# Performance work log

Measured on AMD Instinct MI355X. Metric: run time of the kernel, lower is better.

Reference implementation:

```python
import jax, jax.numpy as jnp
import numpy as np

B = 16384
ED = 32          # embed_dim
NF = 16          # num_filters
KS = [1, 3, 5, 7, 9]
LENS = {"pep": 12, "a1": 7, "a2": 8, "a3": 22, "b1": 6, "b2": 7, "b3": 23}


def setup_inputs() -> dict:
    key = jax.random.key(0)
    keys = jax.random.split(key, 32)
    ki = iter(keys)
    inp = {}
    for name, L in LENS.items():
        inp[name] = jax.random.normal(next(ki), (B, ED, L), dtype=jnp.float32)
    # conv weights: one stack of 7 convs per kernel size; w{k}: [7, NF, ED, k], bias c{k}: [7, NF]
    for k in KS:
        fan_in = ED * k
        bound = 1.0 / np.sqrt(fan_in)
        inp[f"w{k}"] = jax.random.uniform(next(ki), (7, NF, ED, k), jnp.float32, -bound, bound)
        inp[f"c{k}"] = jax.random.uniform(next(ki), (7, NF), jnp.float32, -bound, bound)
    dbound = 1.0 / np.sqrt(NF * 35)
    inp["dw"] = jax.random.uniform(next(ki), (NF * 35, 1), jnp.float32, -dbound, dbound)
    inp["db"] = jax.random.uniform(next(ki), (1,), jnp.float32, -dbound, dbound)
    return inp


def _branch(x, w, b):
    # x: [B, ED, L], w: [NF, ED, k], b: [NF] -> [B, NF] (conv 'same' + relu + global max)
    y = jax.lax.conv_general_dilated(x, w, window_strides=(1,), padding="SAME",
                                     dimension_numbers=("NCH", "OIH", "NCH"))
    y = jax.nn.relu(y + b[None, :, None])
    return jnp.max(y, axis=2)


def reference(pep, a1, a2, a3, b1, b2, b3, w1, w3, w5, w7, w9, c1, c3, c5, c7, c9, dw, db):
    xs = [pep, a1, a2, a3, b1, b2, b3]
    ws = {1: w1, 3: w3, 5: w5, 7: w7, 9: w9}
    cs = {1: c1, 3: c3, 5: c5, 7: c7, 9: c9}
    feats = []
    for i, x in enumerate(xs):  # fixed 7 inputs
        for k in KS:            # fixed 5 kernel sizes
            feats.append(_branch(x, ws[k][i], cs[k][i]))
    feat = jnp.concatenate(feats, axis=1)        # [B, 35*NF]
    out = jax.nn.sigmoid(feat @ dw + db)         # [B, 1]
    return jnp.squeeze(out, axis=-1)             # [B]
```

## Files before the change

### kernel.cpp

```cpp
#include <hip/hip_runtime.h>
#include <cmath>

namespace {

using bf16x8 = __attribute__((ext_vector_type(8))) short;
using f32x4  = __attribute__((ext_vector_type(4))) float;

constexpr int NT = 192;
constexpr int NS = 16;
constexpr int LPAD = 31;
constexpr int TILE_BYTES = NS * LPAD * 32 * 2;

__device__ __forceinline__ short f2bf(float f) {
  unsigned u = __float_as_uint(f);
  unsigned r = (u + 0x7FFFu + ((u >> 16) & 1u)) >> 16;
  return (short)r;
}

__device__ __forceinline__ int gidx(int s, int q, int cq) {
  return (s * 31 + q) * 4 + ((cq ^ ((s >> 1) + (q >> 1))) & 3);
}

__device__ __forceinline__ bf16x8 ldcol(const char* smem, int s, int cq, int q) {
  return *(const bf16x8*)(smem + (gidx(s, q, cq) << 4));
}

template<int K1, int K2>
__device__ __forceinline__ void run_role(
    const char* __restrict__ smem, int s, int cq, int f,
    const float* __restrict__ wk1, const float* __restrict__ ck1,
    const float* __restrict__ wk2, const float* __restrict__ ck2,
    const float* __restrict__ dw, int i, int L, f32x4& dvec)
{
  constexpr int KK1 = (K1 - 1) / 2;
  constexpr int KK2 = (K2 > 0) ? (K2 - 1) / 2 : 0;

  bf16x8 wf1[K1];
  #pragma unroll
  for (int t = 0; t < K1; ++t) {
    const float* wp = wk1 + (size_t)((i * 16 + f) * 32 + cq * 8) * K1 + t;
    bf16x8 v;
    #pragma unroll
    for (int j = 0; j < 8; ++j) v[j] = f2bf(wp[(size_t)j * K1]);
    wf1[t] = v;
  }
  bf16x8 wf2[(K2 > 0) ? K2 : 1];
  if constexpr (K2 > 0) {
    #pragma unroll
    for (int t = 0; t < K2; ++t) {
      const float* wp = wk2 + (size_t)((i * 16 + f) * 32 + cq * 8) * K2 + t;
      bf16x8 v;
      #pragma unroll
      for (int j = 0; j < 8; ++j) v[j] = f2bf(wp[(size_t)j * K2]);
      wf2[t] = v;
    }
  }

  const float b1 = ck1[i * 16 + f];
  float b2 = 0.f;
  if constexpr (K2 > 0) b2 = ck2[i * 16 + f];

  f32x4 mx1 = {0.f, 0.f, 0.f, 0.f};
  f32x4 mx2 = {0.f, 0.f, 0.f, 0.f};

  bf16x8 af[K1];
  #pragma unroll
  for (int j = 0; j < K1; ++j) af[j] = ldcol(smem, s, cq, 4 - KK1 + j);

  auto body = [&](int p, int pi) {
    f32x4 aa = {b1, b1, b1, b1};
    f32x4 ab = {0.f, 0.f, 0.f, 0.f};
    #pragma unroll
    for (int t = 0; t < K1; ++t) {
      if (t & 1)
        ab = __builtin_amdgcn_mfma_f32_16x16x32_bf16(af[(pi + t) % K1], wf1[t], ab, 0, 0, 0);
      else
        aa = __builtin_amdgcn_mfma_f32_16x16x32_bf16(af[(pi + t) % K1], wf1[t], aa, 0, 0, 0);
    }
    if constexpr (K2 > 0) {
      f32x4 ac = {b2, b2, b2, b2};
      #pragma unroll
      for (int t = 0; t < K2; ++t)
        ac = __builtin_amdgcn_mfma_f32_16x16x32_bf16(af[(pi + (KK1 - KK2) + t) % K1], wf2[t], ac, 0, 0, 0);
      #pragma unroll
      for (int r = 0; r < 4; ++r) mx2[r] = fmaxf(mx2[r], ac[r]);
    }
    #pragma unroll
    for (int r = 0; r < 4; ++r) mx1[r] = fmaxf(mx1[r], aa[r] + ab[r]);
    if (p + pi + 1 < L)
      af[pi] = ldcol(smem, s, cq, p + pi + 5 + KK1);
  };

  int p = 0;
  for (; p + K1 <= L; p += K1) {
    #pragma unroll
    for (int pi = 0; pi < K1; ++pi) body(p, pi);
  }
  #pragma unroll
  for (int pi = 0; pi < K1 - 1; ++pi)
    if (p + pi < L) body(p, pi);

  {
    const float dv1 = dw[(i * 5 + KK1) * 16 + f];
    #pragma unroll
    for (int r = 0; r < 4; ++r) dvec[r] = fmaf(mx1[r], dv1, dvec[r]);
  }
  if constexpr (K2 > 0) {
    const float dv2 = dw[(i * 5 + KK2) * 16 + f];
    #pragma unroll
    for (int r = 0; r < 4; ++r) dvec[r] = fmaf(mx2[r], dv2, dvec[r]);
  }
}

__global__ __launch_bounds__(NT, 3) void nettcr_mfma(
    const float* __restrict__ x0, const float* __restrict__ x1,
    const float* __restrict__ x2, const float* __restrict__ x3,
    const float* __restrict__ x4, const float* __restrict__ x5,
    const float* __restrict__ x6,
    const float* __restrict__ w1, const float* __restrict__ c1,
    const float* __restrict__ w3, const float* __restrict__ c3,
    const float* __restrict__ w5, const float* __restrict__ c5,
    const float* __restrict__ w7, const float* __restrict__ c7,
    const float* __restrict__ w9, const float* __restrict__ c9,
    const float* __restrict__ dw, const float* __restrict__ db,
    float* __restrict__ out)
{
  __shared__ __align__(16) char smem[TILE_BYTES];
  const int tid  = threadIdx.x;
  const int lane = tid & 63;
  const int wid  = tid >> 6;
  const int s    = lane & 15;
  const int cq   = lane >> 4;
  const int f    = lane & 15;
  const int b0   = blockIdx.x * NS;

  f32x4 dvec = {0.f, 0.f, 0.f, 0.f};

  for (int i = 0; i < 7; ++i) {
    const float* xi; int L;
    switch (i) {
      case 0: xi = x0; L = 12; break;
      case 1: xi = x1; L = 7;  break;
      case 2: xi = x2; L = 8;  break;
      case 3: xi = x3; L = 22; break;
      case 4: xi = x4; L = 6;  break;
      case 5: xi = x5; L = 7;  break;
      default: xi = x6; L = 23; break;
    }
    __syncthreads();
    for (int e = tid; e < 64 * L; e += NT) {
      const int l  = e % L;
      const int rr = e / L;
      const int cg = rr & 3;
      const int ss = rr >> 2;
      const float* src = xi + ((size_t)(b0 + ss) * 32 + cg * 8) * L + l;
      bf16x8 pk;
      #pragma unroll
      for (int j = 0; j < 8; ++j) pk[j] = f2bf(src[(size_t)j * L]);
      *(bf16x8*)(smem + (gidx(ss, l + 4, cg) << 4)) = pk;
    }
    for (int e = tid; e < 512; e += NT) {
      const int q8 = e & 7;
      const int q  = (q8 < 4) ? q8 : (L + q8);
      const int cg = (e >> 3) & 3;
      const int ss = e >> 5;
      bf16x8 z = {0, 0, 0, 0, 0, 0, 0, 0};
      *(bf16x8*)(smem + (gidx(ss, q, cg) << 4)) = z;
    }
    __syncthreads();

    if (wid == 0)
      run_role<9, 0>(smem, s, cq, f, w9, c9, nullptr, nullptr, dw, i, L, dvec);
    else if (wid == 1)
      run_role<7, 1>(smem, s, cq, f, w7, c7, w1, c1, dw, i, L, dvec);
    else
      run_role<5, 3>(smem, s, cq, f, w5, c5, w3, c3, dw, i, L, dvec);
  }

  __syncthreads();
  float* red = (float*)smem;
  *(f32x4*)&red[(wid * 64 + lane) * 4] = dvec;
  __syncthreads();
  if (tid < 16) {
    float sum = db[0];
    const int g4 = tid >> 2, r = tid & 3;
    for (int w = 0; w < 3; ++w)
      #pragma unroll
      for (int f2 = 0; f2 < 16; ++f2)
        sum += red[(w * 64 + g4 * 16 + f2) * 4 + r];
    out[b0 + tid] = 1.0f / (1.0f + expf(-sum));
  }
}

}

extern "C" void kernel_launch(void* const* d_in, const int* in_sizes, int n_in,
                              void* d_out, int out_size, void* d_ws, size_t ws_size,
                              hipStream_t stream) {
  (void)d_ws; (void)ws_size; (void)out_size;
  const float* xs[7];
  for (int i = 0; i < 7; ++i) xs[i] = (const float*)d_in[i];

  const float* wptr[5] = {nullptr, nullptr, nullptr, nullptr, nullptr};
  const float* cptr[5] = {nullptr, nullptr, nullptr, nullptr, nullptr};
  const float* dw = nullptr;
  const float* db = nullptr;
  int c_seen = 0;
  for (int idx = 7; idx < n_in; ++idx) {
    const int sz = in_sizes[idx];
    const float* p = (const float*)d_in[idx];
    if (sz == 1) { db = p; }
    else if (sz == 16 * 35) { dw = p; }
    else if (sz == 7 * 16) { cptr[c_seen++] = p; }
    else {
      const int k = sz / (7 * 16 * 32);
      wptr[(k - 1) / 2] = p;
    }
  }

  float* out = (float*)d_out;
  const int B = 16384;
  dim3 grid(B / NS), block(NT);
  hipLaunchKernelGGL(nettcr_mfma, grid, block, 0, stream,
                     xs[0], xs[1], xs[2], xs[3], xs[4], xs[5], xs[6],
                     wptr[0], cptr[0], wptr[1], cptr[1], wptr[2], cptr[2],
                     wptr[3], cptr[3], wptr[4], cptr[4], dw, db, out);
}
```

Before: 98.56 us.

## Pre-pack bf16 weights, vectorize input staging, and specialize per-input loops at compile time

Adds a small pre-kernel that converts the conv weights into bf16 MFMA fragments once per call in workspace, so each block loads packed 16-byte granules instead of strided scalar float loads plus conversion. Input staging now reads four consecutive positions per thread with vector loads. Each input is processed by a template instantiation with compile-time length, which fully unrolls the sliding loops. The change also alters the LDS swizzle and raises launch bounds to 4 waves per SIMD. Costs are an extra kernel launch and possible register pressure from the higher occupancy target and the unrolling.

```diff
diff --git a/kernel.cpp b/kernel.cpp
--- a/kernel.cpp
+++ b/kernel.cpp
@@ -5,60 +5,93 @@
 
 using bf16x8 = __attribute__((ext_vector_type(8))) short;
 using f32x4  = __attribute__((ext_vector_type(4))) float;
+using f32x4u = __attribute__((ext_vector_type(4), aligned(4))) float;
 
 constexpr int NT = 192;
 constexpr int NS = 16;
 constexpr int LPAD = 31;
 constexpr int TILE_BYTES = NS * LPAD * 32 * 2;
 
+constexpr int WOFF1 = 0, WOFF3 = 448, WOFF5 = 1792, WOFF7 = 4032, WOFF9 = 7168;
+constexpr int WGRANULES = 11200;
+
 __device__ __forceinline__ short f2bf(float f) {
   unsigned u = __float_as_uint(f);
-  unsigned r = (u + 0x7FFFu + ((u >> 16) & 1u)) >> 16;
-  return (short)r;
+  return (short)((u + 0x7FFFu + ((u >> 16) & 1u)) >> 16);
 }
 
 __device__ __forceinline__ int gidx(int s, int q, int cq) {
-  return (s * 31 + q) * 4 + ((cq ^ ((s >> 1) + (q >> 1))) & 3);
+  return (s * 31 + q) * 4 + ((cq ^ (s >> 1) ^ (q >> 1)) & 3);
 }
 
 __device__ __forceinline__ bf16x8 ldcol(const char* smem, int s, int cq, int q) {
   return *(const bf16x8*)(smem + (gidx(s, q, cq) << 4));
 }
 
-template<int K1, int K2>
+template<int L>
+__device__ __forceinline__ void stage_tile(const float* __restrict__ xi,
+                                           char* __restrict__ smem, int tid, int b0) {
+  constexpr int L4 = (L + 3) / 4;
+  const bf16x8 z = {0, 0, 0, 0, 0, 0, 0, 0};
+  #pragma unroll
+  for (int e0 = 0; e0 < 512; e0 += NT) {
+    const int e = e0 + tid;
+    if (e < 512) {
+      const int q8 = e & 7;
+      const int q  = (q8 < 4) ? q8 : (L + q8);
+      const int cg = (e >> 3) & 3;
+      const int ss = e >> 5;
+      *(bf16x8*)(smem + (gidx(ss, q, cg) << 4)) = z;
+    }
+  }
+  #pragma unroll
+  for (int e0 = 0; e0 < 64 * L4; e0 += NT) {
+    const int e = e0 + tid;
+    if (e < 64 * L4) {
+      const int l4 = e % L4;
+      const int rr = e / L4;
+      const int cg = rr & 3;
+      const int ss = rr >> 2;
+      const int l0 = (l4 == L4 - 1) ? (L - 4) : (l4 * 4);
+      const float* src = xi + ((size_t)(b0 + ss) * 32 + cg * 8) * L + l0;
+      f32x4u v[8];
+      #pragma unroll
+      for (int j = 0; j < 8; ++j) v[j] = *(const f32x4u*)(src + (size_t)j * L);
+      #pragma unroll
+      for (int p = 0; p < 4; ++p) {
+        bf16x8 pk;
+        #pragma unroll
+        for (int j = 0; j < 8; ++j) pk[j] = f2bf(v[j][p]);
+        *(bf16x8*)(smem + (gidx(ss, l0 + 4 + p, cg) << 4)) = pk;
+      }
+    }
+  }
+}
+
+template<int K1, int K2, int I, int L>
 __device__ __forceinline__ void run_role(
     const char* __restrict__ smem, int s, int cq, int f,
-    const float* __restrict__ wk1, const float* __restrict__ ck1,
-    const float* __restrict__ wk2, const float* __restrict__ ck2,
-    const float* __restrict__ dw, int i, int L, f32x4& dvec)
+    const bf16x8* __restrict__ wg1, const float* __restrict__ ck1,
+    const bf16x8* __restrict__ wg2, const float* __restrict__ ck2,
+    const float* __restrict__ dw, f32x4& dvec)
 {
   constexpr int KK1 = (K1 - 1) / 2;
   constexpr int KK2 = (K2 > 0) ? (K2 - 1) / 2 : 0;
 
   bf16x8 wf1[K1];
   #pragma unroll
-  for (int t = 0; t < K1; ++t) {
-    const float* wp = wk1 + (size_t)((i * 16 + f) * 32 + cq * 8) * K1 + t;
-    bf16x8 v;
-    #pragma unroll
-    for (int j = 0; j < 8; ++j) v[j] = f2bf(wp[(size_t)j * K1]);
-    wf1[t] = v;
-  }
+  for (int t = 0; t < K1; ++t)
+    wf1[t] = wg1[((I * 16 + f) * 4 + cq) * K1 + t];
   bf16x8 wf2[(K2 > 0) ? K2 : 1];
   if constexpr (K2 > 0) {
     #pragma unroll
-    for (int t = 0; t < K2; ++t) {
-      const float* wp = wk2 + (size_t)((i * 16 + f) * 32 + cq * 8) * K2 + t;
-      bf16x8 v;
-      #pragma unroll
-      for (int j = 0; j < 8; ++j) v[j] = f2bf(wp[(size_t)j * K2]);
-      wf2[t] = v;
-    }
-  }
-
-  const float b1 = ck1[i * 16 + f];
+    for (int t = 0; t < K2; ++t)
+      wf2[t] = wg2[((I * 16 + f) * 4 + cq) * K2 + t];
+  }
+
+  const float b1 = ck1[I * 16 + f];
   float b2 = 0.f;
-  if constexpr (K2 > 0) b2 = ck2[i * 16 + f];
+  if constexpr (K2 > 0) b2 = ck2[I * 16 + f];
 
   f32x4 mx1 = {0.f, 0.f, 0.f, 0.f};
   f32x4 mx2 = {0.f, 0.f, 0.f, 0.f};
@@ -91,91 +124,102 @@
       af[pi] = ldcol(smem, s, cq, p + pi + 5 + KK1);
   };
 
-  int p = 0;
-  for (; p + K1 <= L; p += K1) {
+  #pragma unroll
+  for (int p = 0; p + K1 <= L; p += K1) {
     #pragma unroll
     for (int pi = 0; pi < K1; ++pi) body(p, pi);
   }
+  constexpr int PB = (L / K1) * K1;
   #pragma unroll
   for (int pi = 0; pi < K1 - 1; ++pi)
-    if (p + pi < L) body(p, pi);
+    if (PB + pi < L) body(PB, pi);
 
   {
-    const float dv1 = dw[(i * 5 + KK1) * 16 + f];
+    const float dv1 = dw[(I * 5 + KK1) * 16 + f];
     #pragma unroll
     for (int r = 0; r < 4; ++r) dvec[r] = fmaf(mx1[r], dv1, dvec[r]);
   }
   if constexpr (K2 > 0) {
-    const float dv2 = dw[(i * 5 + KK2) * 16 + f];
+    const float dv2 = dw[(I * 5 + KK2) * 16 + f];
     #pragma unroll
     for (int r = 0; r < 4; ++r) dvec[r] = fmaf(mx2[r], dv2, dvec[r]);
   }
 }
 
-__global__ __launch_bounds__(NT, 3) void nettcr_mfma(
+template<int I, int L>
+__device__ __forceinline__ void process_input(
+    const float* __restrict__ xi, char* __restrict__ smem,
+    int tid, int wid, int lane, int b0,
+    const bf16x8* __restrict__ wg,
+    const float* __restrict__ c1, const float* __restrict__ c3,
+    const float* __restrict__ c5, const float* __restrict__ c7,
+    const float* __restrict__ c9, const float* __restrict__ dw,
+    f32x4& dvec)
+{
+  const int s  = lane & 15;
+  const int cq = lane >> 4;
+  const int f  = lane & 15;
+  __syncthreads();
+  stage_tile<L>(xi, smem, tid, b0);
+  __syncthreads();
+  if (wid == 0)
+    run_role<9, 0, I, L>(smem, s, cq, f, wg + WOFF9, c9, nullptr, nullptr, dw, dvec);
+  else if (wid == 1)
+    run_role<7, 1, I, L>(smem, s, cq, f, wg + WOFF7, c7, wg + WOFF1, c1, dw, dvec);
+  else
+    run_role<5, 3, I, L>(smem, s, cq, f, wg + WOFF5, c5, wg + WOFF3, c3, dw, dvec);
+}
+
+__global__ void prep_weights(const float* __restrict__ w1, const float* __restrict__ w3,
+                             const float* __restrict__ w5, const float* __restrict__ w7,
+                             const float* __restrict__ w9, bf16x8* __restrict__ out)
+{
+  const int g = blockIdx.x * blockDim.x + threadIdx.x;
+  if (g >= WGRANULES) return;
+  int k, base; const float* w;
+  if (g < WOFF3)      { k = 1; base = WOFF1; w = w1; }
+  else if (g < WOFF5) { k = 3; base = WOFF3; w = w3; }
+  else if (g < WOFF7) { k = 5; base = WOFF5; w = w5; }
+  else if (g < WOFF9) { k = 7; base = WOFF7; w = w7; }
+  else                { k = 9; base = WOFF9; w = w9; }
+  const int r  = g - base;
+  const int t  = r % k;
+  const int u  = r / k;
+  const int fi = u >> 2;
+  const int cg = u & 3;
+  bf16x8 v;
+  #pragma unroll
+  for (int j = 0; j < 8; ++j)
+    v[j] = f2bf(w[(size_t)(fi * 32 + cg * 8 + j) * k + t]);
+  out[g] = v;
+}
+
+__global__ __launch_bounds__(NT, 4) void nettcr_mfma(
     const float* __restrict__ x0, const float* __restrict__ x1,
     const float* __restrict__ x2, const float* __restrict__ x3,
     const float* __restrict__ x4, const float* __restrict__ x5,
     const float* __restrict__ x6,
-    const float* __restrict__ w1, const float* __restrict__ c1,
-    const float* __restrict__ w3, const float* __restrict__ c3,
-    const float* __restrict__ w5, const float* __restrict__ c5,
-    const float* __restrict__ w7, const float* __restrict__ c7,
-    const float* __restrict__ w9, const float* __restrict__ c9,
+    const float* __restrict__ c1, const float* __restrict__ c3,
+    const float* __restrict__ c5, const float* __restrict__ c7,
+    const float* __restrict__ c9,
     const float* __restrict__ dw, const float* __restrict__ db,
+    const bf16x8* __restrict__ wg,
     float* __restrict__ out)
 {
   __shared__ __align__(16) char smem[TILE_BYTES];
   const int tid  = threadIdx.x;
   const int lane = tid & 63;
   const int wid  = tid >> 6;
-  const int s    = lane & 15;
-  const int cq   = lane >> 4;
-  const int f    = lane & 15;
   const int b0   = blockIdx.x * NS;
 
   f32x4 dvec = {0.f, 0.f, 0.f, 0.f};
-
-  for (int i = 0; i < 7; ++i) {
-    const float* xi; int L;
-    switch (i) {
-      case 0: xi = x0; L = 12; break;
-      case 1: xi = x1; L = 7;  break;
-      case 2: xi = x2; L = 8;  break;
-      case 3: xi = x3; L = 22; break;
-      case 4: xi = x4; L = 6;  break;
-      case 5: xi = x5; L = 7;  break;
-      default: xi = x6; L = 23; break;
-    }
-    __syncthreads();
-    for (int e = tid; e < 64 * L; e += NT) {
-      const int l  = e % L;
-      const int rr = e / L;
-      const int cg = rr & 3;
-      const int ss = rr >> 2;
-      const float* src = xi + ((size_t)(b0 + ss) * 32 + cg * 8) * L + l;
-      bf16x8 pk;
-      #pragma unroll
-      for (int j = 0; j < 8; ++j) pk[j] = f2bf(src[(size_t)j * L]);
-      *(bf16x8*)(smem + (gidx(ss, l + 4, cg) << 4)) = pk;
-    }
-    for (int e = tid; e < 512; e += NT) {
-      const int q8 = e & 7;
-      const int q  = (q8 < 4) ? q8 : (L + q8);
-      const int cg = (e >> 3) & 3;
-      const int ss = e >> 5;
-      bf16x8 z = {0, 0, 0, 0, 0, 0, 0, 0};
-      *(bf16x8*)(smem + (gidx(ss, q, cg) << 4)) = z;
-    }
-    __syncthreads();
-
-    if (wid == 0)
-      run_role<9, 0>(smem, s, cq, f, w9, c9, nullptr, nullptr, dw, i, L, dvec);
-    else if (wid == 1)
-      run_role<7, 1>(smem, s, cq, f, w7, c7, w1, c1, dw, i, L, dvec);
-    else
-      run_role<5, 3>(smem, s, cq, f, w5, c5, w3, c3, dw, i, L, dvec);
-  }
+  process_input<0, 12>(x0, smem, tid, wid, lane, b0, wg, c1, c3, c5, c7, c9, dw, dvec);
+  process_input<1,  7>(x1, smem, tid, wid, lane, b0, wg, c1, c3, c5, c7, c9, dw, dvec);
+  process_input<2,  8>(x2, smem, tid, wid, lane, b0, wg, c1, c3, c5, c7, c9, dw, dvec);
+  process_input<3, 22>(x3, smem, tid, wid, lane, b0, wg, c1, c3, c5, c7, c9, dw, dvec);
+  process_input<4,  6>(x4, smem, tid, wid, lane, b0, wg, c1, c3, c5, c7, c9, dw, dvec);
+  process_input<5,  7>(x5, smem, tid, wid, lane, b0, wg, c1, c3, c5, c7, c9, dw, dvec);
+  process_input<6, 23>(x6, smem, tid, wid, lane, b0, wg, c1, c3, c5, c7, c9, dw, dvec);
 
   __syncthreads();
   float* red = (float*)smem;
@@ -197,7 +241,7 @@
 extern "C" void kernel_launch(void* const* d_in, const int* in_sizes, int n_in,
                               void* d_out, int out_size, void* d_ws, size_t ws_size,
                               hipStream_t stream) {
-  (void)d_ws; (void)ws_size; (void)out_size;
+  (void)ws_size; (void)out_size;
   const float* xs[7];
   for (int i = 0; i < 7; ++i) xs[i] = (const float*)d_in[i];
 
@@ -218,11 +262,15 @@
     }
   }
 
+  bf16x8* wg = (bf16x8*)d_ws;
+  hipLaunchKernelGGL(prep_weights, dim3((WGRANULES + 255) / 256), dim3(256), 0, stream,
+                     wptr[0], wptr[1], wptr[2], wptr[3], wptr[4], wg);
+
   float* out = (float*)d_out;
   const int B = 16384;
   dim3 grid(B / NS), block(NT);
   hipLaunchKernelGGL(nettcr_mfma, grid, block, 0, stream,
                      xs[0], xs[1], xs[2], xs[3], xs[4], xs[5], xs[6],
-                     wptr[0], cptr[0], wptr[1], cptr[1], wptr[2], cptr[2],
-                     wptr[3], cptr[3], wptr[4], cptr[4], dw, db, out);
-}
+                     cptr[0], cptr[1], cptr[2], cptr[3], cptr[4],
+                     dw, db, wg, out);
+}
```

New measurement: 337.6 us. +242.5%, slower.
